# Optimization experiments

Hardware: AMD Instinct MI355X
Metric: run time of the kernel (lower is better)

## Reference

```python
import jax, jax.numpy as jnp
import numpy as np

# ---- static configuration (mirrors init_kwargs) ----
PAD = 4
C = 5
MODEL_HW = 512
PSF_M = 41
PSF_O = 61
RES_IN = 0.2
RES_OUT = 0.4
PHI = 0.05          # rotation_angle = angle_out - angle_in
FLIP = (1.0, 1.0)   # flip_sign = sign_in * sign_out
OBS_H = OBS_W = 220


def good_fft_size(n):
    # smallest 2^k or 3*2^(k-2) >= n (good radix-2/3 FFT size)
    q = 2 ** int(np.ceil(np.log2(n)))
    if 3 * q // 4 >= n:
        q = 3 * q // 4
    return int(q)


def _pad_center(x, fft_shape, axes=(-2, -1)):
    pads = [(0, 0)] * x.ndim
    for ax, s in zip(axes, fft_shape):
        d = s - x.shape[ax]
        pads[ax] = (d // 2, d - d // 2)
    return jnp.pad(x, pads)


def transform(x, fft_shape, axes=(-2, -1)):
    # centered zero-pad, ifftshift, rfft2 -> (..., N, N//2+1) complex
    xp = jnp.fft.ifftshift(_pad_center(x, fft_shape, axes), axes)
    return jnp.fft.rfftn(xp, axes=axes)


def _bilinear(im, rows, cols):
    # complex bilinear interpolation, zero outside the grid
    ny, nx = im.shape
    r0 = jnp.floor(rows).astype(jnp.int32)
    c0 = jnp.floor(cols).astype(jnp.int32)
    dr = rows - r0
    dc = cols - c0
    def g(r, c):
        ok = (r >= 0) & (r < ny) & (c >= 0) & (c < nx)
        return jnp.where(ok, im[jnp.clip(r, 0, ny - 1), jnp.clip(c, 0, nx - 1)], 0)
    return (g(r0, c0) * (1 - dr) * (1 - dc) + g(r0 + 1, c0) * dr * (1 - dc)
            + g(r0, c0 + 1) * (1 - dr) * dc + g(r0 + 1, c0 + 1) * dr * dc)


def resample_ops(kim, shape_in, shape_out, res_in, res_out, phi=None, flip_sign=None):
    # resample a half-plane (hermitian) kimage onto the target k-grid,
    # with optional rotation / axis-sign flip; uses f(-k) = conj(f(k))
    # for samples that rotate into kx < 0.
    T = shape_out
    ymin = (-T) // 2  # matches -fft_shape_target // 2 convention in the caller
    ky = jnp.arange(T, dtype=jnp.float32) + ymin          # rows after fftshift(-2)
    kx = jnp.arange(T // 2 + 1, dtype=jnp.float32)        # kx >= 0 half-plane
    KX, KY = jnp.meshgrid(kx, ky)                          # (T, T//2+1)
    scale = (shape_in * res_in) / (T * res_out)            # output index -> input index
    fx, fy = KX * scale, KY * scale
    if flip_sign is not None:
        fx = fx * flip_sign[0]
        fy = fy * flip_sign[1]
    if phi is not None:
        cs, sn = jnp.cos(phi), jnp.sin(phi)
        fx, fy = cs * fx - sn * fy, sn * fx + cs * fy
    neg = fx < 0
    fxs = jnp.where(neg, -fx, fx)
    fys = jnp.where(neg, -fy, fy)
    rows = fys + shape_in // 2  # input rows are fftshifted: ky_in = i - N//2
    cols = fxs
    vals = jax.vmap(lambda im: _bilinear(im, rows, cols))(kim)
    return jnp.where(neg[None], jnp.conj(vals), vals)


def _wrap_hermitian_x(im, im_xmin, im_ymin, wrap_xmin, wrap_ymin, wrap_nx, wrap_ny):
    # expand half-plane to full plane via hermitian symmetry, periodically
    # wrap (accumulate) every sample into the target region, contract back.
    ny, nxh = im.shape
    full = jnp.concatenate([jnp.conj(im[:, 1:])[::-1, ::-1], im], axis=1)  # x: -(nxh-1)..nxh-1
    xs = jnp.arange(full.shape[1]) - (nxh - 1)
    ys = jnp.arange(ny) + im_ymin
    col = (xs - wrap_xmin) % wrap_nx + wrap_xmin + (nxh - 1)
    row = (ys - wrap_ymin) % wrap_ny + wrap_ymin - im_ymin
    out = jnp.zeros_like(full).at[row[:, None], col[None, :]].add(full)
    return out[:, nxh - 1:]


def _trim(x, shape):
    sl = tuple(slice((cs - s) // 2, (cs - s) // 2 + s) for cs, s in zip(x.shape, shape))
    return x[sl]


def setup_inputs() -> dict:
    key = jax.random.key(0)
    model = jax.random.uniform(key, (C, MODEL_HW, MODEL_HW), jnp.float32)
    def gauss_psf(n, sigma):
        r = jnp.arange(n, dtype=jnp.float32) - (n - 1) / 2
        g = jnp.exp(-0.5 * (r[:, None] ** 2 + r[None, :] ** 2) / sigma ** 2)
        g = g / g.sum()
        return jnp.tile(g[None], (C, 1, 1)).astype(jnp.float32)
    # well-conditioned PSFs (required: model PSF is deconvolved in k-space)
    psf_model = gauss_psf(PSF_M, 0.8)
    psf_obs = gauss_psf(PSF_O, 2.5)
    return {"model": model, "psf_model": psf_model, "psf_obs": psf_obs}


def reference(model, psf_model, psf_obs):
    n_im = good_fft_size(PAD * max(model.shape[-2:]))      # 2048
    n_pm = good_fft_size(PAD * max(psf_model.shape[-2:]))  # 192
    n_po = good_fft_size(PAD * max(psf_obs.shape[-2:]))    # 256
    T = min(n_im, n_po) + 1                                # 257
    # k-space PSFs (precomputed in __init__ in the original)
    model_kpsf = jnp.fft.fftshift(transform(psf_model, (n_pm, n_pm)), axes=-2)
    obs_kpsf = jnp.fft.fftshift(transform(psf_obs, (n_po, n_po)), axes=-2)
    model_kpsf_i = resample_ops(model_kpsf, n_pm, T, RES_IN, RES_OUT, PHI, FLIP)
    obs_kpsf_i = resample_ops(obs_kpsf, n_po, T, RES_OUT, RES_OUT)
    # forward path
    model_kim = jnp.fft.fftshift(transform(model, (n_im, n_im)), axes=-2)
    model_kim_i = resample_ops(model_kim, n_im, T, RES_IN, RES_OUT, PHI, FLIP)
    kfinal = model_kim_i / model_kpsf_i * obs_kpsf_i       # deconvolve/convolve
    wmin = (-T) // 2
    kwrap = jax.vmap(_wrap_hermitian_x, in_axes=(0, None, None, None, None, None, None))(
        kfinal, wmin, wmin, wmin + 1, wmin, T - 1, T - 1)
    kwrap = kwrap[:, :-1, :]                               # (C, T-1, T//2+1)
    kshift = jnp.fft.ifftshift(kwrap, axes=(-2,))
    real = jnp.fft.fftshift(jnp.fft.irfft2(kshift, (T - 1, T - 1), (-2, -1)), axes=(-2, -1))
    return _trim(real, (model.shape[0], OBS_H, OBS_W))
```

## Files before the change

kernel.cpp:

```cpp
#include <hip/hip_runtime.h>

#define CC   5
#define MHW  512
#define NIM  2048
#define R_LO 488
#define NRM  1088
#define NCM  576

#define PSM  41
#define NPM  192
#define PR_LO 40
#define PNR  112
#define PNC  56

#define PSO  61
#define NPO  256
#define NCO  129

#define TT   257
#define KXN  129
#define OBS  220

#define DPI 3.14159265358979323846264338327950288
#define PIF 3.14159265358979f

static __device__ __forceinline__ float2 cmulf2(float2 a, float2 b) {
    return make_float2(a.x * b.x - a.y * b.y, a.x * b.y + a.y * b.x);
}

__global__ __launch_bounds__(256) void fft_row(const float* __restrict__ A,
                                               float2* __restrict__ T1r) {
    __shared__ float2 Ab[512];
    __shared__ float2 Bb[512];
    __shared__ float2 tw[256];
    __shared__ float2 outw[NCM];
    int tid = threadIdx.x;
    int row = blockIdx.x;
    {
        float th = (float)tid * (-2.0f * PIF / 512.0f);
        float s, c; __sincosf(th, &s, &c);
        tw[tid] = make_float2(c, s);
    }
    float r0 = A[(size_t)row * 512 + tid];
    float r1 = A[(size_t)row * 512 + 256 + tid];
    __syncthreads();
    for (int v = 0; v < 4; v++) {
        {
            float th0 = (float)(v * tid) * (-2.0f * PIF / 2048.0f);
            float th1 = (float)(v * (tid + 256)) * (-2.0f * PIF / 2048.0f);
            float s0, c0, s1, c1;
            __sincosf(th0, &s0, &c0);
            __sincosf(th1, &s1, &c1);
            Ab[tid]       = make_float2(r0 * c0, r0 * s0);
            Ab[tid + 256] = make_float2(r1 * c1, r1 * s1);
        }
        __syncthreads();
        float2 *src = Ab, *dst = Bb;
        #pragma unroll
        for (int s = 0; s < 9; s++) {
            int Ns = 1 << s;
            int jm = tid & (Ns - 1);
            float2 v0 = src[tid];
            float2 v1 = cmulf2(tw[jm << (8 - s)], src[tid + 256]);
            int idxD = ((tid >> s) << (s + 1)) + jm;
            dst[idxD]      = make_float2(v0.x + v1.x, v0.y + v1.y);
            dst[idxD + Ns] = make_float2(v0.x - v1.x, v0.y - v1.y);
            float2* t = src; src = dst; dst = t;
            __syncthreads();
        }
        if (tid < 144) outw[4 * tid + v] = src[tid];
        __syncthreads();
    }
    for (int c = tid; c < NCM; c += 256)
        T1r[(size_t)row * NCM + c] = outw[c];
}

__global__ __launch_bounds__(256) void fft_col(const float2* __restrict__ T1r,
                                               float2* __restrict__ Fmt) {
    __shared__ float2 Ab[512];
    __shared__ float2 Bb[512];
    __shared__ float2 tw[256];
    __shared__ float2 outw[1088];
    int tid = threadIdx.x;
    int col = blockIdx.x;
    int ch = col / NCM, n = col - ch * NCM;
    {
        float th = (float)tid * (-2.0f * PIF / 512.0f);
        float s, c; __sincosf(th, &s, &c);
        tw[tid] = make_float2(c, s);
    }
    float2 x0 = T1r[((size_t)ch * 512 + tid) * NCM + n];
    float2 x1 = T1r[((size_t)ch * 512 + 256 + tid) * NCM + n];
    __syncthreads();
    for (int v = 0; v < 4; v++) {
        {
            float th0 = (float)(v * tid) * (-2.0f * PIF / 2048.0f);
            float th1 = (float)(v * (tid + 256)) * (-2.0f * PIF / 2048.0f);
            float s0, c0, s1, c1;
            __sincosf(th0, &s0, &c0);
            __sincosf(th1, &s1, &c1);
            Ab[tid]       = cmulf2(make_float2(c0, s0), x0);
            Ab[tid + 256] = cmulf2(make_float2(c1, s1), x1);
        }
        __syncthreads();
        float2 *src = Ab, *dst = Bb;
        #pragma unroll
        for (int s = 0; s < 9; s++) {
            int Ns = 1 << s;
            int jm = tid & (Ns - 1);
            float2 v0 = src[tid];
            float2 v1 = cmulf2(tw[jm << (8 - s)], src[tid + 256]);
            int idxD = ((tid >> s) << (s + 1)) + jm;
            dst[idxD]      = make_float2(v0.x + v1.x, v0.y + v1.y);
            dst[idxD + Ns] = make_float2(v0.x - v1.x, v0.y - v1.y);
            float2* t = src; src = dst; dst = t;
            __syncthreads();
        }
        #pragma unroll
        for (int h = 0; h < 2; h++) {
            int u = tid + h * 256;
            int kr = 4 * u + v;
            if (kr <= 551)       outw[kr + 536]  = src[u];
            else if (kr >= 1512) outw[kr - 1512] = src[u];
        }
        __syncthreads();
    }
    for (int m = tid; m < 1088; m += 256)
        Fmt[(size_t)col * 1088 + m] = outw[m];
}

#define M1B 45
#define O1B 154
__global__ __launch_bounds__(256) void psf_s1(const float* __restrict__ psfm,
                                              const float* __restrict__ psfo,
                                              float2* __restrict__ Tp,
                                              float2* __restrict__ To) {
    __shared__ float2 t192s[NPM];
    __shared__ float2 t256s[NPO];
    int tid = threadIdx.x;
    for (int t = tid; t < NPM; t += 256) {
        double a = -2.0 * DPI * (double)t / (double)NPM;
        t192s[t] = make_float2((float)cos(a), (float)sin(a));
    }
    {
        double a = -2.0 * DPI * (double)tid / (double)NPO;
        t256s[tid] = make_float2((float)cos(a), (float)sin(a));
    }
    __syncthreads();
    int b = blockIdx.x;
    if (b < M1B) {
        int idx = b * 256 + tid;
        if (idx >= CC * PSM * PNC) return;
        int c = idx % PNC, y = (idx / PNC) % PSM, ch = idx / (PNC * PSM);
        const float* p = psfm + (ch * PSM + y) * PSM;
        float2 acc = make_float2(0.f, 0.f);
        for (int x = 0; x < PSM; x++) {
            float2 w = t192s[(c * x) % NPM];
            float v = p[x];
            acc.x = fmaf(v, w.x, acc.x);
            acc.y = fmaf(v, w.y, acc.y);
        }
        Tp[idx] = acc;
    } else {
        int idx = (b - M1B) * 256 + tid;
        if (idx >= CC * PSO * NCO) return;
        int c = idx % NCO, y = (idx / NCO) % PSO, ch = idx / (NCO * PSO);
        const float* p = psfo + (ch * PSO + y) * PSO;
        float2 acc = make_float2(0.f, 0.f);
        for (int x = 0; x < PSO; x++) {
            float2 w = t256s[(c * x) & (NPO - 1)];
            float v = p[x];
            acc.x = fmaf(v, w.x, acc.x);
            acc.y = fmaf(v, w.y, acc.y);
        }
        To[idx] = acc;
    }
}

#define M2B 123
#define O2B 645
__global__ __launch_bounds__(256) void psf_s2(const float2* __restrict__ Tp,
                                              const float2* __restrict__ To,
                                              float2* __restrict__ Fp,
                                              float2* __restrict__ Fo) {
    __shared__ float2 t192s[NPM];
    __shared__ float2 t256s[NPO];
    int tid = threadIdx.x;
    for (int t = tid; t < NPM; t += 256) {
        double a = -2.0 * DPI * (double)t / (double)NPM;
        t192s[t] = make_float2((float)cos(a), (float)sin(a));
    }
    {
        double a = -2.0 * DPI * (double)tid / (double)NPO;
        t256s[tid] = make_float2((float)cos(a), (float)sin(a));
    }
    __syncthreads();
    int b = blockIdx.x;
    if (b < M2B) {
        int idx = b * 256 + tid;
        if (idx >= CC * PNR * PNC) return;
        int c = idx % PNC, rr = (idx / PNC) % PNR, ch = idx / (PNC * PNR);
        int ky = rr + (PR_LO - 96);
        const float2* t = Tp + (ch * PSM) * PNC + c;
        float2 acc = make_float2(0.f, 0.f);
        for (int y = 0; y < PSM; y++) {
            int tt = (ky * y) % NPM; if (tt < 0) tt += NPM;
            float2 w = t192s[tt];
            float2 v = t[y * PNC];
            acc.x = fmaf(v.x, w.x, acc.x); acc.x = fmaf(-v.y, w.y, acc.x);
            acc.y = fmaf(v.x, w.y, acc.y); acc.y = fmaf(v.y, w.x, acc.y);
        }
        Fp[idx] = acc;
    } else {
        int idx = (b - M2B) * 256 + tid;
        if (idx >= CC * NPO * NCO) return;
        int c = idx % NCO, r = (idx / NCO) % NPO, ch = idx / (NCO * NPO);
        int ky = r - 128;
        const float2* t = To + (ch * PSO) * NCO + c;
        float2 acc = make_float2(0.f, 0.f);
        for (int y = 0; y < PSO; y++) {
            float2 w = t256s[(ky * y) & (NPO - 1)];
            float2 v = t[y * NCO];
            acc.x = fmaf(v.x, w.x, acc.x); acc.x = fmaf(-v.y, w.y, acc.x);
            acc.y = fmaf(v.x, w.y, acc.y); acc.y = fmaf(v.y, w.x, acc.y);
        }
        Fo[idx] = acc;
    }
}

__global__ __launch_bounds__(256) void sampler(const float2* __restrict__ Fmt,
                                               const float2* __restrict__ Fp,
                                               const float2* __restrict__ Fo,
                                               float2* __restrict__ KF) {
    __shared__ float2 t8[8];
    __shared__ float2 t192[NPM];
    __shared__ float2 t256[NPO];
    int tid = threadIdx.x;
    if (tid < 8) {
        double a = 2.0 * DPI * (double)tid / 8.0;
        t8[tid] = make_float2((float)cos(a), (float)sin(a));
    }
    for (int t = tid; t < NPM; t += 256) {
        double a = 2.0 * DPI * (double)t / (double)NPM;
        t192[t] = make_float2((float)cos(a), (float)sin(a));
    }
    {
        double a = 2.0 * DPI * (double)tid / (double)NPO;
        t256[tid] = make_float2((float)cos(a), (float)sin(a));
    }
    __syncthreads();
    int idx = blockIdx.x * 256 + tid;
    if (idx >= CC * TT * KXN) return;
    int j = idx % KXN, i = (idx / KXN) % TT, ch = idx / (KXN * TT);

    float fkx = (float)j;
    float fky = (float)(i - 129);

    const float CS  = (float)0.9987502603949669;
    const float SN  = (float)0.04997916927067832;
    const float SCM = (float)(2048.0 * 0.2 / (257.0 * 0.4));
    const float SCP = (float)(192.0  * 0.2 / (257.0 * 0.4));
    const float SCO = (float)(256.0  * 0.4 / (257.0 * 0.4));

    float2 vm;
    {
        float fx = fkx * SCM, fy = fky * SCM;
        float fxr = CS * fx - SN * fy;
        float fyr = SN * fx + CS * fy;
        bool neg = fxr < 0.0f;
        float fxs = neg ? -fxr : fxr;
        float fys = neg ? -fyr : fyr;
        float rows = fys + 1024.0f, cols = fxs;
        float r0f = floorf(rows), c0f = floorf(cols);
        int r0 = (int)r0f, c0 = (int)c0f;
        float dr = rows - r0f, dc = cols - c0f;
        float2 g[2][2];
        #pragma unroll
        for (int a = 0; a < 2; a++)
            #pragma unroll
            for (int b = 0; b < 2; b++) {
                int r = r0 + a, c = c0 + b;
                float2 v = make_float2(0.f, 0.f);
                if (r >= R_LO && r < R_LO + NRM && c >= 0 && c < NCM) {
                    float2 f = Fmt[((size_t)ch * NCM + c) * NRM + (r - R_LO)];
                    v = cmulf2(t8[(r - 1024 + c) & 7], f);
                }
                g[a][b] = v;
            }
        float w00 = (1.f - dr) * (1.f - dc), w10 = dr * (1.f - dc);
        float w01 = (1.f - dr) * dc,         w11 = dr * dc;
        vm.x = g[0][0].x * w00 + g[1][0].x * w10 + g[0][1].x * w01 + g[1][1].x * w11;
        vm.y = g[0][0].y * w00 + g[1][0].y * w10 + g[0][1].y * w01 + g[1][1].y * w11;
        if (neg) vm.y = -vm.y;
    }

    float2 vp;
    {
        float fx = fkx * SCP, fy = fky * SCP;
        float fxr = CS * fx - SN * fy;
        float fyr = SN * fx + CS * fy;
        bool neg = fxr < 0.0f;
        float fxs = neg ? -fxr : fxr;
        float fys = neg ? -fyr : fyr;
        float rows = fys + 96.0f, cols = fxs;
        float r0f = floorf(rows), c0f = floorf(cols);
        int r0 = (int)r0f, c0 = (int)c0f;
        float dr = rows - r0f, dc = cols - c0f;
        float2 g[2][2];
        #pragma unroll
        for (int a = 0; a < 2; a++)
            #pragma unroll
            for (int b = 0; b < 2; b++) {
                int r = r0 + a, c = c0 + b;
                float2 v = make_float2(0.f, 0.f);
                if (r >= PR_LO && r < PR_LO + PNR && c >= 0 && c < PNC) {
                    float2 f = Fp[((size_t)ch * PNR + (r - PR_LO)) * PNC + c];
                    int k = r - 96 + c;
                    int tph = (21 * k) % NPM; if (tph < 0) tph += NPM;
                    v = cmulf2(t192[tph], f);
                }
                g[a][b] = v;
            }
        float w00 = (1.f - dr) * (1.f - dc), w10 = dr * (1.f - dc);
        float w01 = (1.f - dr) * dc,         w11 = dr * dc;
        vp.x = g[0][0].x * w00 + g[1][0].x * w10 + g[0][1].x * w01 + g[1][1].x * w11;
        vp.y = g[0][0].y * w00 + g[1][0].y * w10 + g[0][1].y * w01 + g[1][1].y * w11;
        if (neg) vp.y = -vp.y;
    }

    float2 vo;
    {
        float fx = fkx * SCO, fy = fky * SCO;
        float rows = fy + 128.0f, cols = fx;
        float r0f = floorf(rows), c0f = floorf(cols);
        int r0 = (int)r0f, c0 = (int)c0f;
        float dr = rows - r0f, dc = cols - c0f;
        float2 g[2][2];
        #pragma unroll
        for (int a = 0; a < 2; a++)
            #pragma unroll
            for (int b = 0; b < 2; b++) {
                int r = r0 + a, c = c0 + b;
                float2 v = make_float2(0.f, 0.f);
                if (r >= 0 && r < NPO && c >= 0 && c < NCO) {
                    float2 f = Fo[((size_t)ch * NPO + r) * NCO + c];
                    int tph = (31 * (r - 128 + c)) & (NPO - 1);
                    v = cmulf2(t256[tph], f);
                }
                g[a][b] = v;
            }
        float w00 = (1.f - dr) * (1.f - dc), w10 = dr * (1.f - dc);
        float w01 = (1.f - dr) * dc,         w11 = dr * dc;
        vo.x = g[0][0].x * w00 + g[1][0].x * w10 + g[0][1].x * w01 + g[1][1].x * w11;
        vo.y = g[0][0].y * w00 + g[1][0].y * w10 + g[0][1].y * w01 + g[1][1].y * w11;
    }

    float den = vp.x * vp.x + vp.y * vp.y;
    float2 q = make_float2((vm.x * vp.x + vm.y * vp.y) / den,
                           (vm.y * vp.x - vm.x * vp.y) / den);
    KF[idx] = cmulf2(q, vo);
}

#define SWZ(t) ((t) ^ (((t) >> 4) & 15))
__global__ __launch_bounds__(512) void inv12(const float2* __restrict__ KF,
                                             float* __restrict__ out) {
    __shared__ float2 t256[NPO];
    __shared__ float2 part[4][128];
    __shared__ float2 arow[128];
    int tid = threadIdx.x;
    if (tid < NPO) {
        double a = 2.0 * DPI * (double)tid / (double)NPO;
        t256[SWZ(tid)] = make_float2((float)cos(a), (float)sin(a));
    }
    __syncthreads();
    int mr = blockIdx.x, ch = blockIdx.y;
    int mp = 146 + mr;
    int kx = tid & 127, q = tid >> 7;
    const float2* base = KF + (size_t)ch * TT * KXN + kx;
    float2 a0 = make_float2(0.f, 0.f), a1 = a0, a2 = a0, a3 = a0;
    int rlo = q * 64;
    #pragma unroll 4
    for (int rr = 0; rr < 64; rr += 4) {
        int r = rlo + rr;
        float2 k0 = base[(size_t)(r + 0) * KXN];
        float2 k1 = base[(size_t)(r + 1) * KXN];
        float2 k2 = base[(size_t)(r + 2) * KXN];
        float2 k3 = base[(size_t)(r + 3) * KXN];
        int i0 = ((r + 0) * mp) & 255;
        int i1 = ((r + 1) * mp) & 255;
        int i2 = ((r + 2) * mp) & 255;
        int i3 = ((r + 3) * mp) & 255;
        float2 w0 = t256[SWZ(i0)], w1 = t256[SWZ(i1)];
        float2 w2 = t256[SWZ(i2)], w3 = t256[SWZ(i3)];
        a0.x = fmaf(k0.x, w0.x, a0.x); a0.x = fmaf(-k0.y, w0.y, a0.x);
        a0.y = fmaf(k0.x, w0.y, a0.y); a0.y = fmaf(k0.y, w0.x, a0.y);
        a1.x = fmaf(k1.x, w1.x, a1.x); a1.x = fmaf(-k1.y, w1.y, a1.x);
        a1.y = fmaf(k1.x, w1.y, a1.y); a1.y = fmaf(k1.y, w1.x, a1.y);
        a2.x = fmaf(k2.x, w2.x, a2.x); a2.x = fmaf(-k2.y, w2.y, a2.x);
        a2.y = fmaf(k2.x, w2.y, a2.y); a2.y = fmaf(k2.y, w2.x, a2.y);
        a3.x = fmaf(k3.x, w3.x, a3.x); a3.x = fmaf(-k3.y, w3.y, a3.x);
        a3.y = fmaf(k3.x, w3.y, a3.y); a3.y = fmaf(k3.y, w3.x, a3.y);
    }
    if (q == 0) {
        float2 fold = base[(size_t)256 * KXN];
        a0.x += fold.x; a0.y += fold.y;
    }
    part[q][kx] = make_float2((a0.x + a1.x) + (a2.x + a3.x),
                              (a0.y + a1.y) + (a2.y + a3.y));
    __syncthreads();
    if (tid < 128) {
        float2 p0 = part[0][tid], p1 = part[1][tid];
        float2 p2 = part[2][tid], p3 = part[3][tid];
        arow[tid] = make_float2((p0.x + p1.x) + (p2.x + p3.x),
                                (p0.y + p1.y) + (p2.y + p3.y));
    }
    __syncthreads();
    if (tid >= OBS) return;
    int np = 146 + tid;
    float s0 = 0.f, s1 = 0.f, s2 = 0.f, s3 = 0.f;
    #pragma unroll 4
    for (int k = 1; k + 3 <= 127; k += 4) {
        float2 v0 = arow[k + 0], v1 = arow[k + 1];
        float2 v2 = arow[k + 2], v3 = arow[k + 3];
        int i0 = ((k + 0) * np) & 255;
        int i1 = ((k + 1) * np) & 255;
        int i2 = ((k + 2) * np) & 255;
        int i3 = ((k + 3) * np) & 255;
        float2 w0 = t256[SWZ(i0)], w1 = t256[SWZ(i1)];
        float2 w2 = t256[SWZ(i2)], w3 = t256[SWZ(i3)];
        s0 = fmaf(v0.x, w0.x, s0); s0 = fmaf(-v0.y, w0.y, s0);
        s1 = fmaf(v1.x, w1.x, s1); s1 = fmaf(-v1.y, w1.y, s1);
        s2 = fmaf(v2.x, w2.x, s2); s2 = fmaf(-v2.y, w2.y, s2);
        s3 = fmaf(v3.x, w3.x, s3); s3 = fmaf(-v3.y, w3.y, s3);
    }
    for (int k = 125; k < 128; k++) {
        float2 v = arow[k];
        int i = (k * np) & 255;
        float2 w = t256[SWZ(i)];
        s0 = fmaf(v.x, w.x, s0); s0 = fmaf(-v.y, w.y, s0);
    }
    float s = arow[0].x + 2.0f * ((s0 + s1) + (s2 + s3));
    s *= (1.0f / 65536.0f);
    if (mr & 1) s = -s;
    out[((size_t)ch * OBS + mr) * OBS + tid] = s;
}

extern "C" void kernel_launch(void* const* d_in, const int* in_sizes, int n_in,
                              void* d_out, int out_size, void* d_ws, size_t ws_size,
                              hipStream_t stream) {
    const float* model = (const float*)d_in[0];
    const float* psfm  = (const float*)d_in[1];
    const float* psfo  = (const float*)d_in[2];
    float* out = (float*)d_out;

    float2* ws = (float2*)d_ws;
    size_t off = 0;
    float2* T1r = ws + off; off += (size_t)CC * MHW * NCM;
    float2* Fmt = ws + off; off += (size_t)CC * NCM * NRM;
    float2* Tp  = ws + off; off += (size_t)CC * PSM * PNC;
    float2* Fp  = ws + off; off += (size_t)CC * PNR * PNC;
    float2* To  = ws + off; off += (size_t)CC * PSO * NCO;
    float2* Fo  = ws + off; off += (size_t)CC * NPO * NCO;
    float2* KF  = ws + off; off += (size_t)CC * TT * KXN;

    fft_row<<<CC * MHW, 256, 0, stream>>>(model, T1r);
    fft_col<<<CC * NCM, 256, 0, stream>>>(T1r, Fmt);

    psf_s1<<<M1B + O1B, 256, 0, stream>>>(psfm, psfo, Tp, To);
    psf_s2<<<M2B + O2B, 256, 0, stream>>>(Tp, To, Fp, Fo);

    sampler<<<(CC * TT * KXN + 255) / 256, 256, 0, stream>>>(Fmt, Fp, Fo, KF);

    inv12<<<dim3(OBS, CC), 512, 0, stream>>>(KF, out);
}
```

Before: 162.2 us.

## Replace radix-2 shared-memory FFT loops with parallel radix-8 Stockham passes

```diff
diff --git a/kernel.cpp b/kernel.cpp
--- a/kernel.cpp
+++ b/kernel.cpp
@@ -23,110 +23,163 @@
 
 #define DPI 3.14159265358979323846264338327950288
 #define PIF 3.14159265358979f
+#define S2F 0.70710678118654752f
 
 static __device__ __forceinline__ float2 cmulf2(float2 a, float2 b) {
     return make_float2(a.x * b.x - a.y * b.y, a.x * b.y + a.y * b.x);
 }
 
+static __device__ __forceinline__ void dft8(const float2 v[8], float2 y[8]) {
+    float2 a0 = make_float2(v[0].x + v[4].x, v[0].y + v[4].y);
+    float2 b0 = make_float2(v[0].x - v[4].x, v[0].y - v[4].y);
+    float2 a1 = make_float2(v[1].x + v[5].x, v[1].y + v[5].y);
+    float2 b1 = make_float2(v[1].x - v[5].x, v[1].y - v[5].y);
+    float2 a2 = make_float2(v[2].x + v[6].x, v[2].y + v[6].y);
+    float2 b2 = make_float2(v[2].x - v[6].x, v[2].y - v[6].y);
+    float2 a3 = make_float2(v[3].x + v[7].x, v[3].y + v[7].y);
+    float2 b3 = make_float2(v[3].x - v[7].x, v[3].y - v[7].y);
+    float2 e0 = make_float2(a0.x + a2.x, a0.y + a2.y);
+    float2 e1 = make_float2(a0.x - a2.x, a0.y - a2.y);
+    float2 f0 = make_float2(a1.x + a3.x, a1.y + a3.y);
+    float2 f1 = make_float2(a1.x - a3.x, a1.y - a3.y);
+    y[0] = make_float2(e0.x + f0.x, e0.y + f0.y);
+    y[4] = make_float2(e0.x - f0.x, e0.y - f0.y);
+    y[2] = make_float2(e1.x + f1.y, e1.y - f1.x);
+    y[6] = make_float2(e1.x - f1.y, e1.y + f1.x);
+    float2 c1 = make_float2(S2F * (b1.x + b1.y), S2F * (b1.y - b1.x));
+    float2 c2 = make_float2(b2.y, -b2.x);
+    float2 c3 = make_float2(S2F * (b3.y - b3.x), -S2F * (b3.x + b3.y));
+    float2 g0 = make_float2(b0.x + c2.x, b0.y + c2.y);
+    float2 g1 = make_float2(b0.x - c2.x, b0.y - c2.y);
+    float2 h0 = make_float2(c1.x + c3.x, c1.y + c3.y);
+    float2 h1 = make_float2(c1.x - c3.x, c1.y - c3.y);
+    y[1] = make_float2(g0.x + h0.x, g0.y + h0.y);
+    y[5] = make_float2(g0.x - h0.x, g0.y - h0.y);
+    y[3] = make_float2(g1.x + h1.y, g1.y - h1.x);
+    y[7] = make_float2(g1.x - h1.y, g1.y + h1.x);
+}
+
+#define SPAD(n) ((n) + ((n) >> 3) + ((n) >> 6))
+#define SSZ 584
+
 __global__ __launch_bounds__(256) void fft_row(const float* __restrict__ A,
                                                float2* __restrict__ T1r) {
-    __shared__ float2 Ab[512];
-    __shared__ float2 Bb[512];
-    __shared__ float2 tw[256];
-    __shared__ float2 outw[NCM];
-    int tid = threadIdx.x;
+    __shared__ float2 BufA[4][SSZ];
+    __shared__ float2 BufB[4][SSZ];
+    float2* outw = &BufA[0][0];
+    float*  xs   = (float*)&BufB[0][0];
+    int tid = threadIdx.x, lane = tid & 63, v = tid >> 6;
     int row = blockIdx.x;
-    {
-        float th = (float)tid * (-2.0f * PIF / 512.0f);
-        float s, c; __sincosf(th, &s, &c);
-        tw[tid] = make_float2(c, s);
-    }
-    float r0 = A[(size_t)row * 512 + tid];
-    float r1 = A[(size_t)row * 512 + 256 + tid];
-    __syncthreads();
-    for (int v = 0; v < 4; v++) {
-        {
-            float th0 = (float)(v * tid) * (-2.0f * PIF / 2048.0f);
-            float th1 = (float)(v * (tid + 256)) * (-2.0f * PIF / 2048.0f);
-            float s0, c0, s1, c1;
-            __sincosf(th0, &s0, &c0);
-            __sincosf(th1, &s1, &c1);
-            Ab[tid]       = make_float2(r0 * c0, r0 * s0);
-            Ab[tid + 256] = make_float2(r1 * c1, r1 * s1);
-        }
-        __syncthreads();
-        float2 *src = Ab, *dst = Bb;
-        #pragma unroll
-        for (int s = 0; s < 9; s++) {
-            int Ns = 1 << s;
-            int jm = tid & (Ns - 1);
-            float2 v0 = src[tid];
-            float2 v1 = cmulf2(tw[jm << (8 - s)], src[tid + 256]);
-            int idxD = ((tid >> s) << (s + 1)) + jm;
-            dst[idxD]      = make_float2(v0.x + v1.x, v0.y + v1.y);
-            dst[idxD + Ns] = make_float2(v0.x - v1.x, v0.y - v1.y);
-            float2* t = src; src = dst; dst = t;
-            __syncthreads();
-        }
-        if (tid < 144) outw[4 * tid + v] = src[tid];
-        __syncthreads();
-    }
-    for (int c = tid; c < NCM; c += 256)
-        T1r[(size_t)row * NCM + c] = outw[c];
+    xs[tid]       = A[(size_t)row * 512 + tid];
+    xs[tid + 256] = A[(size_t)row * 512 + 256 + tid];
+    __syncthreads();
+    float2 vq[8], y[8];
+    float s, c;
+    __sincosf(-2.0f * PIF * (float)(v * lane) / 2048.0f, &s, &c);
+    float2 m = make_float2(c, s);
+    __sincosf(-2.0f * PIF * (float)v / 32.0f, &s, &c);
+    float2 wstep = make_float2(c, s);
+    #pragma unroll
+    for (int q = 0; q < 8; q++) {
+        float xr = xs[q * 64 + lane];
+        vq[q] = make_float2(xr * m.x, xr * m.y);
+        m = cmulf2(m, wstep);
+    }
+    dft8(vq, y);
+    #pragma unroll
+    for (int p = 0; p < 8; p++) BufA[v][SPAD(8 * lane + p)] = y[p];
+    __syncthreads();
+    int jm = lane & 7, g = lane >> 3;
+    __sincosf(-2.0f * PIF * (float)jm / 64.0f, &s, &c);
+    float2 w1 = make_float2(c, s);
+    float2 wq = make_float2(1.f, 0.f);
+    #pragma unroll
+    for (int q = 0; q < 8; q++) {
+        vq[q] = cmulf2(wq, BufA[v][SPAD(lane + q * 64)]);
+        wq = cmulf2(wq, w1);
+    }
+    dft8(vq, y);
+    #pragma unroll
+    for (int p = 0; p < 8; p++) BufB[v][SPAD(g * 64 + jm + p * 8)] = y[p];
+    __syncthreads();
+    __sincosf(-2.0f * PIF * (float)lane / 512.0f, &s, &c);
+    float2 w2 = make_float2(c, s);
+    wq = make_float2(1.f, 0.f);
+    #pragma unroll
+    for (int q = 0; q < 8; q++) {
+        vq[q] = cmulf2(wq, BufB[v][SPAD(lane + q * 64)]);
+        wq = cmulf2(wq, w2);
+    }
+    dft8(vq, y);
+    #pragma unroll
+    for (int p = 0; p < 8; p++) {
+        int u = lane + p * 64;
+        if (u < 144) outw[4 * u + v] = y[p];
+    }
+    __syncthreads();
+    for (int cc = tid; cc < NCM; cc += 256)
+        T1r[(size_t)row * NCM + cc] = outw[cc];
 }
 
 __global__ __launch_bounds__(256) void fft_col(const float2* __restrict__ T1r,
                                                float2* __restrict__ Fmt) {
-    __shared__ float2 Ab[512];
-    __shared__ float2 Bb[512];
-    __shared__ float2 tw[256];
-    __shared__ float2 outw[1088];
-    int tid = threadIdx.x;
+    __shared__ float2 BufA[4][SSZ];
+    __shared__ float2 BufB[4][SSZ];
+    float2* outw = &BufA[0][0];
+    float2* xs   = &BufB[0][0];
+    int tid = threadIdx.x, lane = tid & 63, v = tid >> 6;
     int col = blockIdx.x;
     int ch = col / NCM, n = col - ch * NCM;
-    {
-        float th = (float)tid * (-2.0f * PIF / 512.0f);
-        float s, c; __sincosf(th, &s, &c);
-        tw[tid] = make_float2(c, s);
-    }
-    float2 x0 = T1r[((size_t)ch * 512 + tid) * NCM + n];
-    float2 x1 = T1r[((size_t)ch * 512 + 256 + tid) * NCM + n];
-    __syncthreads();
-    for (int v = 0; v < 4; v++) {
-        {
-            float th0 = (float)(v * tid) * (-2.0f * PIF / 2048.0f);
-            float th1 = (float)(v * (tid + 256)) * (-2.0f * PIF / 2048.0f);
-            float s0, c0, s1, c1;
-            __sincosf(th0, &s0, &c0);
-            __sincosf(th1, &s1, &c1);
-            Ab[tid]       = cmulf2(make_float2(c0, s0), x0);
-            Ab[tid + 256] = cmulf2(make_float2(c1, s1), x1);
-        }
-        __syncthreads();
-        float2 *src = Ab, *dst = Bb;
-        #pragma unroll
-        for (int s = 0; s < 9; s++) {
-            int Ns = 1 << s;
-            int jm = tid & (Ns - 1);
-            float2 v0 = src[tid];
-            float2 v1 = cmulf2(tw[jm << (8 - s)], src[tid + 256]);
-            int idxD = ((tid >> s) << (s + 1)) + jm;
-            dst[idxD]      = make_float2(v0.x + v1.x, v0.y + v1.y);
-            dst[idxD + Ns] = make_float2(v0.x - v1.x, v0.y - v1.y);
-            float2* t = src; src = dst; dst = t;
-            __syncthreads();
-        }
-        #pragma unroll
-        for (int h = 0; h < 2; h++) {
-            int u = tid + h * 256;
-            int kr = 4 * u + v;
-            if (kr <= 551)       outw[kr + 536]  = src[u];
-            else if (kr >= 1512) outw[kr - 1512] = src[u];
-        }
-        __syncthreads();
-    }
-    for (int m = tid; m < 1088; m += 256)
-        Fmt[(size_t)col * 1088 + m] = outw[m];
+    xs[tid]       = T1r[((size_t)ch * 512 + tid) * NCM + n];
+    xs[tid + 256] = T1r[((size_t)ch * 512 + 256 + tid) * NCM + n];
+    __syncthreads();
+    float2 vq[8], y[8];
+    float s, c;
+    __sincosf(-2.0f * PIF * (float)(v * lane) / 2048.0f, &s, &c);
+    float2 m = make_float2(c, s);
+    __sincosf(-2.0f * PIF * (float)v / 32.0f, &s, &c);
+    float2 wstep = make_float2(c, s);
+    #pragma unroll
+    for (int q = 0; q < 8; q++) {
+        vq[q] = cmulf2(m, xs[q * 64 + lane]);
+        m = cmulf2(m, wstep);
+    }
+    dft8(vq, y);
+    #pragma unroll
+    for (int p = 0; p < 8; p++) BufA[v][SPAD(8 * lane + p)] = y[p];
+    __syncthreads();
+    int jm = lane & 7, g = lane >> 3;
+    __sincosf(-2.0f * PIF * (float)jm / 64.0f, &s, &c);
+    float2 w1 = make_float2(c, s);
+    float2 wq = make_float2(1.f, 0.f);
+    #pragma unroll
+    for (int q = 0; q < 8; q++) {
+        vq[q] = cmulf2(wq, BufA[v][SPAD(lane + q * 64)]);
+        wq = cmulf2(wq, w1);
+    }
+    dft8(vq, y);
+    #pragma unroll
+    for (int p = 0; p < 8; p++) BufB[v][SPAD(g * 64 + jm + p * 8)] = y[p];
+    __syncthreads();
+    __sincosf(-2.0f * PIF * (float)lane / 512.0f, &s, &c);
+    float2 w2 = make_float2(c, s);
+    wq = make_float2(1.f, 0.f);
+    #pragma unroll
+    for (int q = 0; q < 8; q++) {
+        vq[q] = cmulf2(wq, BufB[v][SPAD(lane + q * 64)]);
+        wq = cmulf2(wq, w2);
+    }
+    dft8(vq, y);
+    #pragma unroll
+    for (int p = 0; p < 8; p++) {
+        int u = lane + p * 64;
+        int kr = 4 * u + v;
+        if (kr <= 551)       outw[kr + 536]  = y[p];
+        else if (kr >= 1512) outw[kr - 1512] = y[p];
+    }
+    __syncthreads();
+    for (int mm = tid; mm < 1088; mm += 256)
+        Fmt[(size_t)col * 1088 + mm] = outw[mm];
 }
 
 #define M1B 45
```

Result: faster. 135.9 us (-16.2%).
